# Performance work log

Measured on AMD Instinct MI355X. Metric: run time of the kernel, lower is better.

Reference implementation:

```python
import jax, jax.numpy as jnp
import numpy as np
from jax import lax

# Static configuration (matches init_kwargs / input_specs)
B, DIM, H, W = 4, 192, 64, 64
HEADS, SR, WS = 8, 4, 3
HD = DIM // HEADS            # 24
LL = WS * WS                 # 9  (local window length)
N = H * W                    # 4096 tokens
PH, PW = H // SR, W // SR    # 16, 16 pooled grid
PLEN = PH * PW               # 256
PRETRAIN = 512 // 8          # img_size // 2**(i+2) with i=1 -> 64


def _ln(x, g, b, eps=1e-5):
    m = x.mean(-1, keepdims=True)
    v = ((x - m) ** 2).mean(-1, keepdims=True)
    return (x - m) / jnp.sqrt(v + eps) * g + b


def _l2norm(x):
    n = jnp.sqrt(jnp.sum(x * x, -1, keepdims=True))
    return x / jnp.maximum(n, 1e-12)


def _build_static():
    # get_relative_position_cpb: adaptive 1d pool of arange gives key coords
    qh = np.arange(H, dtype=np.float64)
    qw = np.arange(W, dtype=np.float64)
    kh = qh.reshape(PH, SR).mean(-1)  # H divisible by SR -> uniform bins
    kw = qw.reshape(PW, SR).mean(-1)
    KH, KW = np.meshgrid(kh, kw, indexing='ij')
    QH, QW = np.meshgrid(qh, qw, indexing='ij')
    rel_h = (QH.reshape(-1)[:, None] - KH.reshape(-1)[None, :]) / (PRETRAIN - 1) * 8
    rel_w = (QW.reshape(-1)[:, None] - KW.reshape(-1)[None, :]) / (PRETRAIN - 1) * 8
    rel_hw = np.stack([rel_h, rel_w], -1).reshape(-1, 2)
    table, idx = np.unique(rel_hw, axis=0, return_inverse=True)
    table = np.sign(table) * np.log2(np.abs(table) + 1.0) / np.log2(8.0)
    # get_seqlen_and_mask: validity of each of the 9 neighbors per position
    hh, ww = np.meshgrid(np.arange(H), np.arange(W), indexing='ij')
    hh, ww = hh.reshape(-1), ww.reshape(-1)
    valid = np.stack([(hh + dh >= 0) & (hh + dh < H) & (ww + dw >= 0) & (ww + dw < W)
                      for dh in (-1, 0, 1) for dw in (-1, 0, 1)], -1)  # [N, 9]
    pad_mask = ~valid
    seq_scale = np.log(valid.sum(-1, keepdims=True).astype(np.float64) + PLEN).astype(np.float32)  # [N,1]
    return idx.reshape(-1).astype(np.int32), table.astype(np.float32), seq_scale, pad_mask


def setup_inputs() -> dict:
    key = jax.random.key(0)
    ks = jax.random.split(key, 12)
    f32 = jnp.float32

    def tn(k, shape, std=0.02):
        return jax.random.truncated_normal(k, -2.0, 2.0, shape, f32) * std

    rel_idx, table, seq_scale, pad_mask = _build_static()
    return dict(
        x=jax.random.normal(ks[0], (B, DIM, H, W), f32),
        pe_w=tn(ks[1], (DIM, DIM, 3, 3)),
        pe_b=jnp.zeros((DIM,), f32),
        pe_ln_g=jnp.ones((DIM,), f32), pe_ln_b=jnp.zeros((DIM,), f32),
        q_w=tn(ks[2], (DIM, DIM)), q_b=jnp.zeros((DIM,), f32),
        kv_w=tn(ks[3], (2 * DIM, DIM)), kv_b=jnp.zeros((2 * DIM,), f32),
        sr_w=tn(ks[4], (DIM, DIM)), sr_b=jnp.zeros((DIM,), f32),
        norm_g=jnp.ones((DIM,), f32), norm_b=jnp.zeros((DIM,), f32),
        cpb1_w=tn(ks[5], (512, 2), 0.1), cpb1_b=jnp.zeros((512,), f32),
        cpb2_w=tn(ks[6], (HEADS, 512), 0.05), cpb2_b=jnp.zeros((HEADS,), f32),
        rpb_local=tn(ks[7], (HEADS, LL), 0.0004),
        learnable_tokens=tn(ks[8], (HEADS, HD, LL)),
        learnable_bias=jnp.zeros((HEADS, 1, LL), f32),
        query_embedding=tn(ks[9], (HEADS, 1, HD)),
        temperature=jnp.full((HEADS, 1, 1), float(np.log(np.exp(1.0 / 0.24) - 1.0)), f32),
        proj_w=tn(ks[10], (DIM, DIM)), proj_b=jnp.zeros((DIM,), f32),
        out_ln_g=jnp.ones((DIM,), f32), out_ln_b=jnp.zeros((DIM,), f32),
        rel_idx=jnp.asarray(rel_idx),
        coords_table=jnp.asarray(table),
        seq_scale=jnp.asarray(seq_scale),
        pad_mask=jnp.asarray(pad_mask),
    )


def _forward(x, pe_w, pe_b, pe_ln_g, pe_ln_b, q_w, q_b, kv_w, kv_b, sr_w, sr_b,
             norm_g, norm_b, cpb1_w, cpb1_b, cpb2_w, cpb2_b, rpb_local,
             learnable_tokens, learnable_bias, query_embedding, temperature,
             proj_w, proj_b, out_ln_g, out_ln_b,
             rel_idx, coords_table, seq_scale, pad_mask):
    # OverlapPatchEmbed: 3x3 conv s1 p1 -> tokens -> LN
    xc = lax.conv_general_dilated(x, pe_w, (1, 1), ((1, 1), (1, 1)),
                                  dimension_numbers=('NCHW', 'OIHW', 'NCHW')) + pe_b[None, :, None, None]
    t = _ln(xc.reshape(B, DIM, N).transpose(0, 2, 1), pe_ln_g, pe_ln_b)  # [B,N,C]

    # queries
    q = t @ q_w.T + q_b
    q_norm = _l2norm(q.reshape(B, N, HEADS, HD).transpose(0, 2, 1, 3))   # [B,h,N,d]
    q_scaled = (q_norm + query_embedding[None]) * jax.nn.softplus(temperature)[None] * seq_scale

    # local KV via 3x3 neighborhood gather (torch nn.Unfold)
    kv = t @ kv_w.T + kv_b                                               # [B,N,2C]
    k_loc = _l2norm(kv[..., :DIM].reshape(B, N, HEADS, HD)).reshape(B, N, DIM)
    kv_map = jnp.concatenate([k_loc, kv[..., DIM:]], -1).transpose(0, 2, 1).reshape(B, 2 * DIM, H, W)
    p = jnp.pad(kv_map, ((0, 0), (0, 0), (1, 1), (1, 1)))
    neigh = jnp.stack([p[:, :, kh:kh + H, kw:kw + W] for kh in range(WS) for kw in range(WS)], 2)
    neigh = neigh.reshape(B, 2 * HEADS, HD, LL, N).transpose(0, 1, 4, 2, 3)  # [B,2h,N,d,9]
    k_local, v_local = neigh[:, :HEADS], neigh[:, HEADS:]
    attn_local = jnp.einsum('bhnd,bhndl->bhnl', q_scaled, k_local) + rpb_local[None, :, None, :]
    attn_local = jnp.where(pad_mask[None, None], -jnp.inf, attn_local)   # [B,h,N,9]

    # pooled global KV: 1x1 conv -> GELU -> adaptive avg pool -> LN -> kv
    x_map = t.transpose(0, 2, 1).reshape(B, DIM, H, W)
    sr_out = jax.nn.gelu(jnp.einsum('oc,bchw->bohw', sr_w, x_map) + sr_b[None, :, None, None],
                         approximate=False)
    pooled = sr_out.reshape(B, DIM, PH, SR, PW, SR).mean((3, 5)).reshape(B, DIM, PLEN).transpose(0, 2, 1)
    pooled = _ln(pooled, norm_g, norm_b)
    kv_p = (pooled @ kv_w.T + kv_b).reshape(B, PLEN, 2 * HEADS, HD).transpose(0, 2, 1, 3)
    k_pool, v_pool = kv_p[:, :HEADS], kv_p[:, HEADS:]

    # CPB relative position bias for the pooled branch
    cpb = jax.nn.relu(coords_table @ cpb1_w.T + cpb1_b) @ cpb2_w.T + cpb2_b  # [T,h]
    pool_bias = cpb.T[:, rel_idx].reshape(HEADS, N, PLEN)
    attn_pool = jnp.einsum('bhnd,bhmd->bhnm', q_scaled, _l2norm(k_pool)) + pool_bias[None]

    # joint softmax over local + pooled keys
    attn = jax.nn.softmax(jnp.concatenate([attn_local, attn_pool], -1), -1)
    a_loc, a_pool = attn[..., :LL], attn[..., LL:]

    w_loc = jnp.einsum('bhnd,hdl->bhnl', q_norm, learnable_tokens) + learnable_bias[None] + a_loc
    x_local = jnp.einsum('bhnl,bhndl->bhnd', w_loc, v_local)
    x_pool = jnp.einsum('bhnm,bhmd->bhnd', a_pool, v_pool)

    out = (x_local + x_pool).transpose(0, 2, 1, 3).reshape(B, N, DIM) @ proj_w.T + proj_b
    out = _ln(out, out_ln_g, out_ln_b)
    return out.transpose(0, 2, 1).reshape(B, DIM, H, W)


def reference(x, pe_w, pe_b, pe_ln_g, pe_ln_b, q_w, q_b, kv_w, kv_b, sr_w, sr_b,
              norm_g, norm_b, cpb1_w, cpb1_b, cpb2_w, cpb2_b, rpb_local,
              learnable_tokens, learnable_bias, query_embedding, temperature,
              proj_w, proj_b, out_ln_g, out_ln_b,
              rel_idx, coords_table, seq_scale, pad_mask):
    return _forward(x, pe_w, pe_b, pe_ln_g, pe_ln_b, q_w, q_b, kv_w, kv_b, sr_w, sr_b,
                    norm_g, norm_b, cpb1_w, cpb1_b, cpb2_w, cpb2_b, rpb_local,
                    learnable_tokens, learnable_bias, query_embedding, temperature,
                    proj_w, proj_b, out_ln_g, out_ln_b,
                    rel_idx, coords_table, seq_scale, pad_mask)
```

## Files before the change

### kernel.cpp

```cpp
#include <hip/hip_runtime.h>
#include <stdint.h>


__device__ __forceinline__ float b2f(unsigned short u) {
  return __uint_as_float(((unsigned)u) << 16);
}
__device__ __forceinline__ unsigned short f2b(float f) {
  unsigned x = __float_as_uint(f);
  return (unsigned short)((x + 0x7fffu + ((x >> 16) & 1u)) >> 16);
}

constexpr size_t OFF_T    = 0;
constexpr size_t OFF_KMAP = 3145728;
constexpr size_t OFF_QN   = 9437184;
constexpr size_t OFF_QS   = 12582912;
constexpr size_t OFF_CTX  = 15728640;
constexpr size_t OFF_POOL = 18874368;
constexpr size_t OFF_KP   = 19070976;
constexpr size_t OFF_VP   = 19267584;
constexpr size_t OFF_CPB  = 19464192;
constexpr size_t OFF_BIAS = 19595264;
constexpr size_t OFF_WTC  = OFF_CTX;
constexpr size_t OFF_QT   = OFF_CTX + 331776;
constexpr size_t OFF_KVT  = OFF_CTX + 368640;
constexpr size_t OFF_SRT  = OFF_CTX + 442368;
constexpr size_t OFF_PJT  = OFF_KMAP;

__global__ __launch_bounds__(256) void k_wt_all(
    const float* __restrict__ pw, const float* __restrict__ qw,
    const float* __restrict__ kvw, const float* __restrict__ srw,
    float* __restrict__ w) {
  int gb = blockIdx.x;
  int tid = threadIdx.x;
  if (gb < 1296) {
    int i = gb * 256 + tid;
    int j = i % 12;
    int t1 = i / 12;
    int p = t1 % 9;
    int t2 = t1 / 9;
    int ocb = t2 % 16;
    int ic = t2 / 16;
    int oc = ocb * 12 + j;
    w[OFF_WTC + i] = pw[(size_t)oc * 1728 + ic * 9 + p];
  } else if (gb < 1440) {
    int i = (gb - 1296) * 256 + tid;
    int o = i % 192, k = i / 192;
    w[OFF_QT + i] = qw[(size_t)o * 192 + k];
  } else if (gb < 1728) {
    int i = (gb - 1440) * 256 + tid;
    int o = i % 384, k = i / 384;
    w[OFF_KVT + i] = kvw[(size_t)o * 192 + k];
  } else {
    int i = (gb - 1728) * 256 + tid;
    int o = i % 192, k = i / 192;
    w[OFF_SRT + i] = srw[(size_t)o * 192 + k];
  }
}
__global__ __launch_bounds__(256) void k_wt_gen(const float* __restrict__ src,
                                                float* __restrict__ dst, int O, int K) {
  int i = blockIdx.x * 256 + threadIdx.x;
  if (i >= O * K) return;
  int o = i % O, k = i / O;
  dst[i] = src[(size_t)o * K + k];
}

__global__ __launch_bounds__(256) void k_conv(
    const float* __restrict__ x, const float* __restrict__ wtc,
    float* __restrict__ p0, float* __restrict__ p1, float* __restrict__ p2) {
  __shared__ float xl[8 * 6 * 66];
  const int tid = threadIdx.x;
  const int lane = tid & 63;
  const int wv = __builtin_amdgcn_readfirstlane(tid >> 6);
  const int h0 = blockIdx.x * 4;
  const int b = blockIdx.y;
  const int zz = blockIdx.z;
  const int obase = (zz & 3) * 48;
  const int ith = zz >> 2;
  const int icb = ith * 8;
  const int ocb = (zz & 3) * 4 + wv;
  const int ow = obase + wv * 12;

  float acc[4][12];
#pragma unroll
  for (int ro = 0; ro < 4; ++ro)
#pragma unroll
    for (int j = 0; j < 12; ++j) acc[ro][j] = 0.f;

  float xr[13];
  auto loadx = [&](int ic0) {
#pragma unroll
    for (int s = 0; s < 13; ++s) {
      int f = tid + s * 256;
      float v = 0.f;
      if (f < 3168) {
        int ii = f / 396;
        int rem = f - ii * 396;
        int r = rem / 66;
        int wp = rem - r * 66;
        int hh = h0 + r - 1, ww = wp - 1;
        if (hh >= 0 && hh < 64 && ww >= 0 && ww < 64)
          v = x[((size_t)(b * 192 + ic0 * 8 + ii) << 12) + (hh << 6) + ww];
      }
      xr[s] = v;
    }
  };
  loadx(icb);

  for (int i2 = 0; i2 < 8; ++i2) {
    const int ic0 = icb + i2;
    __syncthreads();
#pragma unroll
    for (int s = 0; s < 13; ++s) {
      int f = tid + s * 256;
      if (f < 3168) {
        int ii = f / 396;
        int rem = f - ii * 396;
        int r = rem / 66;
        int wp = rem - r * 66;
        xl[(ii * 6 + r) * 66 + wp] = xr[s];
      }
    }
    __syncthreads();
    if (i2 < 7) loadx(ic0 + 1);
#pragma unroll 1
    for (int ii = 0; ii < 8; ++ii) {
      const float* wb = wtc + ((size_t)((ic0 * 8 + ii) * 16 + ocb) * 9) * 12;
      float xv[6][3];
#pragma unroll
      for (int r6 = 0; r6 < 6; ++r6) {
        const float* xp = &xl[(ii * 6 + r6) * 66 + lane];
        xv[r6][0] = xp[0]; xv[r6][1] = xp[1]; xv[r6][2] = xp[2];
      }
#pragma unroll
      for (int kh = 0; kh < 3; ++kh) {
#pragma unroll
        for (int kw = 0; kw < 3; ++kw) {
          const float4* wp = (const float4*)(wb + (size_t)(kh * 3 + kw) * 12);
          float4 wA = wp[0], wB = wp[1], wC = wp[2];
#pragma unroll
          for (int ro = 0; ro < 4; ++ro) {
            float xvv = xv[ro + kh][kw];
            acc[ro][0]  += xvv * wA.x;
            acc[ro][1]  += xvv * wA.y;
            acc[ro][2]  += xvv * wA.z;
            acc[ro][3]  += xvv * wA.w;
            acc[ro][4]  += xvv * wB.x;
            acc[ro][5]  += xvv * wB.y;
            acc[ro][6]  += xvv * wB.z;
            acc[ro][7]  += xvv * wB.w;
            acc[ro][8]  += xvv * wC.x;
            acc[ro][9]  += xvv * wC.y;
            acc[ro][10] += xvv * wC.z;
            acc[ro][11] += xvv * wC.w;
          }
        }
      }
    }
  }
  float* tdst = (ith == 0) ? p0 : ((ith == 1) ? p1 : p2);
#pragma unroll
  for (int ro = 0; ro < 4; ++ro) {
    float* op = tdst + ((size_t)b * 4096 + (h0 + ro) * 64 + lane) * 192 + ow;
#pragma unroll
    for (int j4 = 0; j4 < 3; ++j4) {
      float4 v;
      v.x = acc[ro][j4 * 4 + 0];
      v.y = acc[ro][j4 * 4 + 1];
      v.z = acc[ro][j4 * 4 + 2];
      v.w = acc[ro][j4 * 4 + 3];
      ((float4*)op)[j4] = v;
    }
  }
}

__global__ __launch_bounds__(256) void k_ln_rows(float* __restrict__ data,
    const float* __restrict__ data2, const float* __restrict__ data3,
    const float* __restrict__ cbias,
    const float* __restrict__ g, const float* __restrict__ be, int rows) {
  int lane = threadIdx.x & 63;
  int wv = threadIdx.x >> 6;
  int row = blockIdx.x * 4 + wv;
  if (row >= rows) return;
  float* p = data + (size_t)row * 192;
  float v0 = p[lane], v1 = p[lane + 64], v2 = p[lane + 128];
  if (data2) {
    const float* q = data2 + (size_t)row * 192;
    v0 += q[lane]; v1 += q[lane + 64]; v2 += q[lane + 128];
  }
  if (data3) {
    const float* q = data3 + (size_t)row * 192;
    v0 += q[lane]; v1 += q[lane + 64]; v2 += q[lane + 128];
  }
  if (cbias) {
    v0 += cbias[lane]; v1 += cbias[lane + 64]; v2 += cbias[lane + 128];
  }
  float s = v0 + v1 + v2;
  float sq = v0 * v0 + v1 * v1 + v2 * v2;
#pragma unroll
  for (int m = 32; m >= 1; m >>= 1) {
    s += __shfl_xor(s, m, 64);
    sq += __shfl_xor(sq, m, 64);
  }
  float mean = s * (1.f / 192.f);
  float var = sq * (1.f / 192.f) - mean * mean;
  float rstd = rsqrtf(var + 1e-5f);
  p[lane]       = (v0 - mean) * rstd * g[lane]       + be[lane];
  p[lane + 64]  = (v1 - mean) * rstd * g[lane + 64]  + be[lane + 64];
  p[lane + 128] = (v2 - mean) * rstd * g[lane + 128] + be[lane + 128];
}

template <int OCB, typename GXV, typename GXD>
__device__ __forceinline__ void gemm_tiles(
    float* __restrict__ xs, int tid, int lane, int wv,
    const float* __restrict__ wt, int ostr, int obase,
    float (&acc)[OCB / 4], GXV gxv, GXD gxd) {
  constexpr int NW4 = OCB / 16;
  float xr[8];
  auto loadx = [&](int k0) {
#pragma unroll
    for (int s = 0; s < 8; ++s) xr[s] = gxv(k0, tid + s * 256);
  };
  loadx(0);
  for (int kt = 0; kt < 6; ++kt) {
    __syncthreads();
#pragma unroll
    for (int s = 0; s < 8; ++s) xs[gxd(tid + s * 256)] = xr[s];
    __syncthreads();
    if (kt < 5) loadx((kt + 1) * 32);
    const float* wbase = wt + (size_t)kt * 32 * ostr + obase + wv * (NW4 * 4);
#pragma unroll 4
    for (int kk = 0; kk < 32; ++kk) {
      float xv = xs[kk * 66 + lane];
      const float4* wrow = (const float4*)(wbase + (size_t)kk * ostr);
#pragma unroll
      for (int j4 = 0; j4 < NW4; ++j4) {
        float4 w4 = wrow[j4];
        acc[j4 * 4 + 0] += xv * w4.x;
        acc[j4 * 4 + 1] += xv * w4.y;
        acc[j4 * 4 + 2] += xv * w4.z;
        acc[j4 * 4 + 3] += xv * w4.w;
      }
    }
  }
}

__global__ __launch_bounds__(256) void k_q(
    const float* __restrict__ t, const float* __restrict__ qt, const float* __restrict__ qb,
    const float* __restrict__ qe, const float* __restrict__ tmp, const float* __restrict__ ss,
    float* __restrict__ qno, float* __restrict__ qso) {
  __shared__ float xs[32 * 66];
  const int tid = threadIdx.x;
  const int lane = tid & 63;
  const int wv = __builtin_amdgcn_readfirstlane(tid >> 6);
  const int n0 = blockIdx.x * 64;
  const int b = blockIdx.y;
  const int obase = blockIdx.z * 96;
  const int hh = blockIdx.z * 4 + wv;
  const int oc0 = obase + wv * 24;
  float acc[24];
#pragma unroll
  for (int j = 0; j < 24; ++j) acc[j] = 0.f;

  gemm_tiles<96>(xs, tid, lane, wv, qt, 192, obase, acc,
    [&](int k0, int f) {
      int nl = f >> 5, kk = f & 31;
      return t[((size_t)b * 4096 + n0 + nl) * 192 + k0 + kk];
    },
    [&](int f) { return (f & 31) * 66 + (f >> 5); });

  const int n = n0 + lane;
  float ssv = ss[n];
  float sumsq = 0.f;
#pragma unroll
  for (int d = 0; d < 24; ++d) {
    float v = acc[d] + qb[oc0 + d];
    sumsq += v * v;
  }
  float rn = 1.f / fmaxf(sqrtf(sumsq), 1e-12f);
  float sp = log1pf(__expf(tmp[hh]));
#pragma unroll
  for (int d = 0; d < 24; ++d) {
    float qv = (acc[d] + qb[oc0 + d]) * rn;
    size_t o = ((size_t)(b * 8 + hh) * 24 + d) * 4096 + n;
    qno[o] = qv;
    qso[o] = (qv + qe[hh * 24 + d]) * sp * ssv;
  }
}

__global__ __launch_bounds__(256) void k_kv(
    const float* __restrict__ t, const float* __restrict__ kvt, const float* __restrict__ kb_,
    float* __restrict__ kmap) {
  __shared__ float xs[32 * 66];
  const int tid = threadIdx.x;
  const int lane = tid & 63;
  const int wv = __builtin_amdgcn_readfirstlane(tid >> 6);
  const int n0 = blockIdx.x * 64;
  const int b = blockIdx.y;
  const int obase = blockIdx.z * 96;
  const int oc0 = obase + wv * 24;
  const int n = n0 + lane;
  float acc[24];
#pragma unroll
  for (int j = 0; j < 24; ++j) acc[j] = 0.f;

  gemm_tiles<96>(xs, tid, lane, wv, kvt, 384, obase, acc,
    [&](int k0, int f) {
      int nl = f >> 5, kk = f & 31;
      return t[((size_t)b * 4096 + n0 + nl) * 192 + k0 + kk];
    },
    [&](int f) { return (f & 31) * 66 + (f >> 5); });

  if (oc0 < 192) {
    float sumsq = 0.f;
#pragma unroll
    for (int d = 0; d < 24; ++d) {
      float v = acc[d] + kb_[oc0 + d];
      sumsq += v * v;
    }
    float rn = 1.f / fmaxf(sqrtf(sumsq), 1e-12f);
#pragma unroll
    for (int d = 0; d < 24; ++d)
      kmap[((size_t)b * 384 + oc0 + d) * 4096 + n] = (acc[d] + kb_[oc0 + d]) * rn;
  } else {
#pragma unroll
    for (int d = 0; d < 24; ++d)
      kmap[((size_t)b * 384 + oc0 + d) * 4096 + n] = acc[d] + kb_[oc0 + d];
  }
}

__device__ __forceinline__ float gelu_exact(float v) {
  float u = v * 0.70710678118654752f;
  float a = fabsf(u);
  float tt = 1.f / (1.f + 0.3275911f * a);
  float poly = ((((1.061405429f * tt - 1.453152027f) * tt + 1.421413741f) * tt
                 - 0.284496736f) * tt + 0.254829592f) * tt;
  float erfa = 1.f - poly * __expf(-a * a);
  float erfv = (u < 0.f) ? -erfa : erfa;
  return 0.5f * v * (1.f + erfv);
}

__global__ __launch_bounds__(256) void k_srpool(
    const float* __restrict__ t, const float* __restrict__ srt, const float* __restrict__ sb,
    float* __restrict__ pooled) {
  __shared__ float xs[32 * 66];
  const int tid = threadIdx.x;
  const int lane = tid & 63;
  const int wv = __builtin_amdgcn_readfirstlane(tid >> 6);
  const int wx = blockIdx.x & 3;
  const int obase = (blockIdx.x >> 2) * 48;
  const int ph = blockIdx.y;
  const int b = blockIdx.z;
  const int oc0 = obase + wv * 12;
  float acc[12];
#pragma unroll
  for (int j = 0; j < 12; ++j) acc[j] = 0.f;

  gemm_tiles<48>(xs, tid, lane, wv, srt, 192, obase, acc,
    [&](int k0, int f) {
      int pl = f >> 5, kk = f & 31;
      int row = (ph * 4 + (pl >> 4)) * 64 + wx * 16 + (pl & 15);
      return t[((size_t)b * 4096 + row) * 192 + k0 + kk];
    },
    [&](int f) { return (f & 31) * 66 + (f >> 5); });

#pragma unroll
  for (int j = 0; j < 12; ++j) {
    float gv = gelu_exact(acc[j] + sb[oc0 + j]);
    gv += __shfl_xor(gv, 1, 64);
    gv += __shfl_xor(gv, 2, 64);
    gv += __shfl_xor(gv, 16, 64);
    gv += __shfl_xor(gv, 32, 64);
    if ((lane & 51) == 0) {
      int cell = (lane >> 2) & 3;
      int p = ph * 16 + wx * 4 + cell;
      pooled[((size_t)b * 256 + p) * 192 + oc0 + j] = gv * (1.f / 16.f);
    }
  }
}

__global__ __launch_bounds__(256) void k_kvp(
    const float* __restrict__ pooled, const float* __restrict__ kvt, const float* __restrict__ kb_,
    float* __restrict__ kp, float* __restrict__ vp) {
  __shared__ float xs[32 * 66];
  const int tid = threadIdx.x;
  const int lane = tid & 63;
  const int wv = __builtin_amdgcn_readfirstlane(tid >> 6);
  const int r0 = blockIdx.x * 64;
  const int obase = blockIdx.y * 96;
  const int oc0 = obase + wv * 24;
  const int row = r0 + lane;
  const int b = row >> 8;
  const int m = row & 255;
  float acc[24];
#pragma unroll
  for (int j = 0; j < 24; ++j) acc[j] = 0.f;

  gemm_tiles<96>(xs, tid, lane, wv, kvt, 384, obase, acc,
    [&](int k0, int f) {
      int nl = f >> 5, kk = f & 31;
      return pooled[(size_t)(r0 + nl) * 192 + k0 + kk];
    },
    [&](int f) { return (f & 31) * 66 + (f >> 5); });

  if (oc0 < 192) {
    int hh = oc0 / 24;
    float sumsq = 0.f;
#pragma unroll
    for (int d = 0; d < 24; ++d) {
      float v = acc[d] + kb_[oc0 + d];
      sumsq += v * v;
    }
    float rn = 1.f / fmaxf(sqrtf(sumsq), 1e-12f);
#pragma unroll
    for (int d = 0; d < 24; ++d)
      kp[(((size_t)(b * 8 + hh)) * 256 + m) * 24 + d] = (acc[d] + kb_[oc0 + d]) * rn;
  } else {
    int hh = (oc0 - 192) / 24;
#pragma unroll
    for (int d = 0; d < 24; ++d)
      vp[(((size_t)(b * 8 + hh)) * 256 + m) * 24 + d] = acc[d] + kb_[oc0 + d];
  }
}

__global__ __launch_bounds__(256) void k_cpb(
    const float* __restrict__ coords, const float* __restrict__ c1w,
    const float* __restrict__ c1b, const float* __restrict__ c2w,
    const float* __restrict__ c2b, float* __restrict__ cpb, int T) {
  __shared__ float s1w[1024];
  __shared__ float s1b[512];
  __shared__ __align__(16) float s2w[512 * 8];
  const int tid = threadIdx.x;
  for (int f = tid; f < 1024; f += 256) s1w[f] = c1w[f];
  for (int f = tid; f < 512; f += 256) s1b[f] = c1b[f];
  for (int f = tid; f < 4096; f += 256) {
    int h = f >> 9, j = f & 511;
    s2w[j * 8 + h] = c2w[f];
  }
  __syncthreads();
  int i = blockIdx.x * 256 + tid;
  int ic = (i < T) ? i : (T - 1);
  float x0 = coords[2 * ic], y0 = coords[2 * ic + 1];
  float a[8];
#pragma unroll
  for (int h = 0; h < 8; ++h) a[h] = c2b[h];
#pragma unroll 4
  for (int j = 0; j < 512; ++j) {
    float hv = fmaxf(s1w[2 * j] * x0 + s1w[2 * j + 1] * y0 + s1b[j], 0.f);
    const float4* w2 = (const float4*)&s2w[j * 8];
    float4 wA = w2[0], wB = w2[1];
    a[0] += hv * wA.x; a[1] += hv * wA.y; a[2] += hv * wA.z; a[3] += hv * wA.w;
    a[4] += hv * wB.x; a[5] += hv * wB.y; a[6] += hv * wB.z; a[7] += hv * wB.w;
  }
  if (i < T) {
#pragma unroll
    for (int h = 0; h < 8; ++h) cpb[(size_t)i * 8 + h] = a[h];
  }
}

__global__ __launch_bounds__(256) void k_bias(
    const int* __restrict__ rel, const float* __restrict__ cpb,
    unsigned short* __restrict__ bt) {
  int g = blockIdx.x * 256 + threadIdx.x;
  int n = g >> 5;
  int m0 = (g & 31) * 8;
  const int4* r4 = (const int4*)(rel + (size_t)n * 256 + m0);
  int4 ra = r4[0], rb = r4[1];
  int idxs[8] = {ra.x, ra.y, ra.z, ra.w, rb.x, rb.y, rb.z, rb.w};
  unsigned acc[8][4];
#pragma unroll
  for (int j = 0; j < 8; ++j) {
    const float4* c4 = (const float4*)(cpb + (size_t)idxs[j] * 8);
    float4 A = c4[0], Bv = c4[1];
    float vals[8] = {A.x, A.y, A.z, A.w, Bv.x, Bv.y, Bv.z, Bv.w};
#pragma unroll
    for (int hh = 0; hh < 8; ++hh) {
      unsigned u = f2b(vals[hh]);
      if (j & 1) acc[hh][j >> 1] |= u << 16;
      else       acc[hh][j >> 1]  = u;
    }
  }
#pragma unroll
  for (int hh = 0; hh < 8; ++hh) {
    uint4 o;
    o.x = acc[hh][0]; o.y = acc[hh][1]; o.z = acc[hh][2]; o.w = acc[hh][3];
    *(uint4*)(bt + ((size_t)hh * 4096 + n) * 256 + m0) = o;
  }
}

__global__ __launch_bounds__(512, 4) void k_attn(
    const float* __restrict__ qs_g, const float* __restrict__ qn_g,
    const float* __restrict__ kmap, const float* __restrict__ kp, const float* __restrict__ vp,
    const unsigned short* __restrict__ bt, const float* __restrict__ rpb,
    const float* __restrict__ lt, const float* __restrict__ lb,
    float* __restrict__ ctx) {
  __shared__ __align__(16) float smem[12288];
  float* kl = smem;
  float* vl = smem + 6144;
  const int tid = threadIdx.x;
  const int lane = tid & 63;
  const int w = __builtin_amdgcn_readfirstlane(tid >> 6);
  const int qm = w & 3;
  const int rr = w >> 2;
  const int row = blockIdx.x * 2 + rr;
  const int h = blockIdx.y;
  const int b = blockIdx.z;
  const int n = (row << 6) + lane;
  const float SHIFT = 15.f;

  {
    const float4* kps = (const float4*)(kp + (size_t)(b * 8 + h) * 6144);
    const float4* vps = (const float4*)(vp + (size_t)(b * 8 + h) * 6144);
    float4* kld = (float4*)kl;
    float4* vld = (float4*)vl;
#pragma unroll
    for (int c = 0; c < 3; ++c) {
      int f = tid + c * 512;
      kld[f] = kps[f];
      vld[f] = vps[f];
    }
  }

  float qsv[24];
  {
    const float* qsb = qs_g + ((size_t)(b * 8 + h) * 24) * 4096 + n;
#pragma unroll
    for (int d = 0; d < 24; ++d) qsv[d] = qsb[(size_t)d * 4096];
  }

  const int l0 = (qm == 1) ? 0 : ((qm == 0) ? 3 : (qm * 2 + 1));
  const int lcnt = (qm == 1) ? 3 : 2;

  float wlv[3];
  {
    float qnv[24];
    const float* qnb = qn_g + ((size_t)(b * 8 + h) * 24) * 4096 + n;
#pragma unroll
    for (int d = 0; d < 24; ++d) qnv[d] = qnb[(size_t)d * 4096];
    const float* ltp = lt + h * 216;
    const float* lbp = lb + h * 9;
#pragma unroll
    for (int j = 0; j < 3; ++j) {
      float a = 0.f;
      if (j < lcnt) {
        int l = l0 + j;
#pragma unroll
        for (int d = 0; d < 24; ++d) a += qnv[d] * ltp[d * 9 + l];
        a += lbp[l];
      }
      wlv[j] = a;
    }
  }

  float ctxA[24], ctxBP[24];
#pragma unroll
  for (int d = 0; d < 24; ++d) { ctxA[d] = 0.f; ctxBP[d] = 0.f; }
  float S = 0.f;

  {
    const float* kbase = kmap + ((size_t)b * 384 + h * 24) * 4096;
    const float* rpp = rpb + h * 9;
    for (int j = 0; j < lcnt; ++j) {
      const int l = l0 + j;
      const int dh = l / 3 - 1, dw = l % 3 - 1;
      const int hp = row + dh;
      if (hp < 0 || hp >= 64) continue;
      const int wp2 = lane + dw;
      const bool okw = (wp2 >= 0) && (wp2 < 64);
      const int nn = (hp << 6) + (okw ? wp2 : lane);
      const float* kb = kbase + nn;
      const float* vb = kb + (size_t)192 * 4096;
      float d0 = 0, d1 = 0, d2 = 0, d3 = 0;
#pragma unroll
      for (int d = 0; d < 24; d += 4) {
        d0 += qsv[d] * kb[(size_t)d * 4096];
        d1 += qsv[d + 1] * kb[(size_t)(d + 1) * 4096];
        d2 += qsv[d + 2] * kb[(size_t)(d + 2) * 4096];
        d3 += qsv[d + 3] * kb[(size_t)(d + 3) * 4096];
      }
      float p = okw ? __expf((d0 + d1) + (d2 + d3) + rpp[l] - SHIFT) : 0.f;
      S += p;
      float wll = okw ? wlv[j] : 0.f;
#pragma unroll
      for (int d = 0; d < 24; ++d) {
        float vv = vb[(size_t)d * 4096];
        ctxA[d] += wll * vv;
        ctxBP[d] += p * vv;
      }
    }
  }

  __syncthreads();

  {
    const unsigned short* bp = bt + ((size_t)h * 4096 + n) * 256 + qm * 64;
    const float* klq = kl + qm * (64 * 24);
    const float* vlq = vl + qm * (64 * 24);
    uint4 bcur = *(const uint4*)bp;
#pragma unroll 1
    for (int c = 0; c < 8; ++c) {
      uint4 bnx = bcur;
      if (c < 7) bnx = *(const uint4*)(bp + (c + 1) * 8);
#pragma unroll
      for (int j = 0; j < 8; ++j) {
        const float4* kr4 = (const float4*)&klq[(c * 8 + j) * 24];
        const float4* vr4 = (const float4*)&vlq[(c * 8 + j) * 24];
        float d0 = 0, d1 = 0, d2 = 0, d3 = 0;
#pragma unroll
        for (int q4 = 0; q4 < 6; ++q4) {
          float4 k4 = kr4[q4];
          d0 += qsv[q4 * 4 + 0] * k4.x;
          d1 += qsv[q4 * 4 + 1] * k4.y;
          d2 += qsv[q4 * 4 + 2] * k4.z;
          d3 += qsv[q4 * 4 + 3] * k4.w;
        }
        unsigned word = (j < 2) ? bcur.x : (j < 4) ? bcur.y : (j < 6) ? bcur.z : bcur.w;
        float bv = (j & 1) ? __uint_as_float(word & 0xffff0000u)
                           : __uint_as_float(word << 16);
        float p = __expf((d0 + d1) + (d2 + d3) + bv - SHIFT);
        S += p;
#pragma unroll
        for (int q4 = 0; q4 < 6; ++q4) {
          float4 v4 = vr4[q4];
          ctxBP[q4 * 4 + 0] += p * v4.x;
          ctxBP[q4 * 4 + 1] += p * v4.y;
          ctxBP[q4 * 4 + 2] += p * v4.z;
          ctxBP[q4 * 4 + 3] += p * v4.w;
        }
      }
      bcur = bnx;
    }
  }

  for (int src = 1; src < 4; ++src) {
    __syncthreads();
    if (qm == src) {
      float* p = smem + (size_t)(rr * 64 + lane) * 49;
      p[0] = S;
#pragma unroll
      for (int d = 0; d < 24; ++d) { p[1 + d] = ctxA[d]; p[25 + d] = ctxBP[d]; }
    }
    __syncthreads();
    if (qm == 0) {
      const float* p = smem + (size_t)(rr * 64 + lane) * 49;
      S += p[0];
#pragma unroll
      for (int d = 0; d < 24; ++d) { ctxA[d] += p[1 + d]; ctxBP[d] += p[25 + d]; }
    }
  }
  if (qm == 0) {
    const float inv = 1.f / S;
    float* cb = ctx + ((size_t)(b * 8 + h) * 24) * 4096 + n;
#pragma unroll
    for (int d = 0; d < 24; ++d)
      cb[(size_t)d * 4096] = ctxA[d] + ctxBP[d] * inv;
  }
}

__global__ __launch_bounds__(256) void k_projg(
    const float* __restrict__ ctx, const float* __restrict__ pjt, const float* __restrict__ pb,
    float* __restrict__ pout) {
  __shared__ float xs[32 * 66];
  const int tid = threadIdx.x;
  const int lane = tid & 63;
  const int wv = __builtin_amdgcn_readfirstlane(tid >> 6);
  const int n0 = blockIdx.x * 64;
  const int b = blockIdx.y;
  const int obase = blockIdx.z * 96;
  const int oc0 = obase + wv * 24;
  const int n = n0 + lane;
  float acc[24];
#pragma unroll
  for (int j = 0; j < 24; ++j) acc[j] = 0.f;

  gemm_tiles<96>(xs, tid, lane, wv, pjt, 192, obase, acc,
    [&](int k0, int f) {
      int kk = f >> 6, nl = f & 63;
      return ctx[((size_t)b * 192 + k0 + kk) * 4096 + n0 + nl];
    },
    [&](int f) { return (f >> 6) * 66 + (f & 63); });

#pragma unroll
  for (int d = 0; d < 24; ++d)
    pout[((size_t)b * 192 + oc0 + d) * 4096 + n] = acc[d] + pb[oc0 + d];
}

__global__ __launch_bounds__(256) void k_oln(
    const float* __restrict__ pout, const float* __restrict__ g,
    const float* __restrict__ be, float* __restrict__ out) {
  __shared__ float red[2][4][64];
  const int tid = threadIdx.x;
  const int lane = tid & 63;
  const int wv = __builtin_amdgcn_readfirstlane(tid >> 6);
  const int n0 = blockIdx.x * 64;
  const int b = blockIdx.y;
  const int o0 = wv * 48;
  float v[48];
  float s = 0.f, sq = 0.f;
#pragma unroll
  for (int j = 0; j < 48; ++j) {
    v[j] = pout[((size_t)b * 192 + o0 + j) * 4096 + n0 + lane];
    s += v[j];
    sq += v[j] * v[j];
  }
  red[0][wv][lane] = s;
  red[1][wv][lane] = sq;
  __syncthreads();
  float st = red[0][0][lane] + red[0][1][lane] + red[0][2][lane] + red[0][3][lane];
  float sqt = red[1][0][lane] + red[1][1][lane] + red[1][2][lane] + red[1][3][lane];
  float mean = st * (1.f / 192.f);
  float var = sqt * (1.f / 192.f) - mean * mean;
  float rstd = rsqrtf(var + 1e-5f);
#pragma unroll
  for (int j = 0; j < 48; ++j) {
    int o = o0 + j;
    out[((size_t)b * 192 + o) * 4096 + n0 + lane] = (v[j] - mean) * rstd * g[o] + be[o];
  }
}

extern "C" void kernel_launch(void* const* d_in, const int* in_sizes, int n_in,
                              void* d_out, int out_size, void* d_ws, size_t ws_size,
                              hipStream_t stream) {
  float* w = (float*)d_ws;

  const float* x      = (const float*)d_in[0];
  const float* pe_w   = (const float*)d_in[1];
  const float* pe_b   = (const float*)d_in[2];
  const float* peln_g = (const float*)d_in[3];
  const float* peln_b = (const float*)d_in[4];
  const float* q_w    = (const float*)d_in[5];
  const float* q_b    = (const float*)d_in[6];
  const float* kv_w   = (const float*)d_in[7];
  const float* kv_b   = (const float*)d_in[8];
  const float* sr_w   = (const float*)d_in[9];
  const float* sr_b   = (const float*)d_in[10];
  const float* norm_g = (const float*)d_in[11];
  const float* norm_b = (const float*)d_in[12];
  const float* cpb1w  = (const float*)d_in[13];
  const float* cpb1b  = (const float*)d_in[14];
  const float* cpb2w  = (const float*)d_in[15];
  const float* cpb2b  = (const float*)d_in[16];
  const float* rpb    = (const float*)d_in[17];
  const float* lt     = (const float*)d_in[18];
  const float* lb     = (const float*)d_in[19];
  const float* qe     = (const float*)d_in[20];
  const float* temp   = (const float*)d_in[21];
  const float* proj_w = (const float*)d_in[22];
  const float* proj_b = (const float*)d_in[23];
  const float* oln_g  = (const float*)d_in[24];
  const float* oln_b  = (const float*)d_in[25];
  const int*   rel    = (const int*)d_in[26];
  const float* coords = (const float*)d_in[27];
  const float* ss     = (const float*)d_in[28];

  dim3 blk(256);
  k_wt_all<<<dim3(1872), blk, 0, stream>>>(pe_w, q_w, kv_w, sr_w, w);

  k_conv<<<dim3(16, 4, 12), blk, 0, stream>>>(x, w + OFF_WTC, w + OFF_T,
      w + OFF_KMAP, w + OFF_KMAP + 3145728);
  k_ln_rows<<<dim3(4096), blk, 0, stream>>>(w + OFF_T, w + OFF_KMAP,
      w + OFF_KMAP + 3145728, pe_b, peln_g, peln_b, 16384);
  k_q<<<dim3(64, 4, 2), blk, 0, stream>>>(w + OFF_T, w + OFF_QT, q_b, qe, temp, ss,
      w + OFF_QN, w + OFF_QS);
  k_kv<<<dim3(64, 4, 4), blk, 0, stream>>>(w + OFF_T, w + OFF_KVT, kv_b, w + OFF_KMAP);
  k_srpool<<<dim3(16, 16, 4), blk, 0, stream>>>(w + OFF_T, w + OFF_SRT, sr_b, w + OFF_POOL);
  k_ln_rows<<<dim3(256), blk, 0, stream>>>(w + OFF_POOL, nullptr, nullptr, nullptr,
      norm_g, norm_b, 1024);
  k_kvp<<<dim3(16, 4), blk, 0, stream>>>(w + OFF_POOL, w + OFF_KVT, kv_b,
      w + OFF_KP, w + OFF_VP);
  int T = in_sizes[27] / 2;
  k_cpb<<<dim3((T + 255) / 256), blk, 0, stream>>>(coords, cpb1w, cpb1b, cpb2w, cpb2b,
      w + OFF_CPB, T);
  k_bias<<<dim3(512), blk, 0, stream>>>(rel, w + OFF_CPB,
      (unsigned short*)(w + OFF_BIAS));
  k_attn<<<dim3(32, 8, 4), dim3(512), 0, stream>>>(w + OFF_QS, w + OFF_QN, w + OFF_KMAP,
      w + OFF_KP, w + OFF_VP, (const unsigned short*)(w + OFF_BIAS), rpb, lt, lb,
      w + OFF_CTX);
  k_wt_gen<<<dim3(144), blk, 0, stream>>>(proj_w, w + OFF_PJT, 192, 192);
  k_projg<<<dim3(64, 4, 2), blk, 0, stream>>>(w + OFF_CTX, w + OFF_PJT, proj_b,
      w + OFF_QN);
  k_oln<<<dim3(64, 4), blk, 0, stream>>>(w + OFF_QN, oln_g, oln_b, (float*)d_out);
}
```

Measured before the change: 546.9 us.

## Fuse output projection with LayerNorm and relayout conv weights to oc-contiguous

Merges the output projection GEMM and the final LayerNorm into one 512-thread kernel, so each block computes all 192 output channels for 64 tokens and normalises them in registers. This removes the intermediate projection write and read-back and one launch. Separately, the patch-embed conv weight transpose now stores weights as [ic*9+p][oc], and the conv kernel indexes with a 192 stride. The fused kernel runs half as many blocks, each twice as large, which may lower occupancy.

```diff
diff --git a/kernel.cpp b/kernel.cpp
--- a/kernel.cpp
+++ b/kernel.cpp
@@ -34,14 +34,8 @@
   int tid = threadIdx.x;
   if (gb < 1296) {
     int i = gb * 256 + tid;
-    int j = i % 12;
-    int t1 = i / 12;
-    int p = t1 % 9;
-    int t2 = t1 / 9;
-    int ocb = t2 % 16;
-    int ic = t2 / 16;
-    int oc = ocb * 12 + j;
-    w[OFF_WTC + i] = pw[(size_t)oc * 1728 + ic * 9 + p];
+    int oc = i % 192, k = i / 192;
+    w[OFF_WTC + i] = pw[(size_t)oc * 1728 + k];
   } else if (gb < 1440) {
     int i = (gb - 1296) * 256 + tid;
     int o = i % 192, k = i / 192;
@@ -77,7 +71,6 @@
   const int obase = (zz & 3) * 48;
   const int ith = zz >> 2;
   const int icb = ith * 8;
-  const int ocb = (zz & 3) * 4 + wv;
   const int ow = obase + wv * 12;
 
   float acc[4][12];
@@ -122,9 +115,9 @@
     }
     __syncthreads();
     if (i2 < 7) loadx(ic0 + 1);
+    const float* wb = wtc + (size_t)ic0 * 72 * 192 + ow;
 #pragma unroll 1
     for (int ii = 0; ii < 8; ++ii) {
-      const float* wb = wtc + ((size_t)((ic0 * 8 + ii) * 16 + ocb) * 9) * 12;
       float xv[6][3];
 #pragma unroll
       for (int r6 = 0; r6 < 6; ++r6) {
@@ -135,7 +128,7 @@
       for (int kh = 0; kh < 3; ++kh) {
 #pragma unroll
         for (int kw = 0; kw < 3; ++kw) {
-          const float4* wp = (const float4*)(wb + (size_t)(kh * 3 + kw) * 12);
+          const float4* wp = (const float4*)(wb + (size_t)(ii * 9 + kh * 3 + kw) * 192);
           float4 wA = wp[0], wB = wp[1], wC = wp[2];
 #pragma unroll
           for (int ro = 0; ro < 4; ++ro) {
@@ -656,64 +649,80 @@
   }
 }
 
-__global__ __launch_bounds__(256) void k_projg(
+__global__ __launch_bounds__(512) void k_projoln(
     const float* __restrict__ ctx, const float* __restrict__ pjt, const float* __restrict__ pb,
-    float* __restrict__ pout) {
+    const float* __restrict__ g, const float* __restrict__ be, float* __restrict__ out) {
   __shared__ float xs[32 * 66];
+  __shared__ float red[2][8][64];
   const int tid = threadIdx.x;
   const int lane = tid & 63;
   const int wv = __builtin_amdgcn_readfirstlane(tid >> 6);
   const int n0 = blockIdx.x * 64;
   const int b = blockIdx.y;
-  const int obase = blockIdx.z * 96;
-  const int oc0 = obase + wv * 24;
-  const int n = n0 + lane;
+  const int oc0 = wv * 24;
   float acc[24];
 #pragma unroll
   for (int j = 0; j < 24; ++j) acc[j] = 0.f;
 
-  gemm_tiles<96>(xs, tid, lane, wv, pjt, 192, obase, acc,
-    [&](int k0, int f) {
+  float xr[4];
+  auto loadx = [&](int k0) {
+#pragma unroll
+    for (int s = 0; s < 4; ++s) {
+      int f = tid + s * 512;
       int kk = f >> 6, nl = f & 63;
-      return ctx[((size_t)b * 192 + k0 + kk) * 4096 + n0 + nl];
-    },
-    [&](int f) { return (f >> 6) * 66 + (f & 63); });
-
-#pragma unroll
-  for (int d = 0; d < 24; ++d)
-    pout[((size_t)b * 192 + oc0 + d) * 4096 + n] = acc[d] + pb[oc0 + d];
-}
-
-__global__ __launch_bounds__(256) void k_oln(
-    const float* __restrict__ pout, const float* __restrict__ g,
-    const float* __restrict__ be, float* __restrict__ out) {
-  __shared__ float red[2][4][64];
-  const int tid = threadIdx.x;
-  const int lane = tid & 63;
-  const int wv = __builtin_amdgcn_readfirstlane(tid >> 6);
-  const int n0 = blockIdx.x * 64;
-  const int b = blockIdx.y;
-  const int o0 = wv * 48;
-  float v[48];
+      xr[s] = ctx[((size_t)b * 192 + k0 + kk) * 4096 + n0 + nl];
+    }
+  };
+  loadx(0);
+  for (int kt = 0; kt < 6; ++kt) {
+    __syncthreads();
+#pragma unroll
+    for (int s = 0; s < 4; ++s) {
+      int f = tid + s * 512;
+      xs[(f >> 6) * 66 + (f & 63)] = xr[s];
+    }
+    __syncthreads();
+    if (kt < 5) loadx((kt + 1) * 32);
+    const float* wbase = pjt + (size_t)kt * 32 * 192 + oc0;
+#pragma unroll 4
+    for (int kk = 0; kk < 32; ++kk) {
+      float xv = xs[kk * 66 + lane];
+      const float4* wrow = (const float4*)(wbase + (size_t)kk * 192);
+#pragma unroll
+      for (int j4 = 0; j4 < 6; ++j4) {
+        float4 w4 = wrow[j4];
+        acc[j4 * 4 + 0] += xv * w4.x;
+        acc[j4 * 4 + 1] += xv * w4.y;
+        acc[j4 * 4 + 2] += xv * w4.z;
+        acc[j4 * 4 + 3] += xv * w4.w;
+      }
+    }
+  }
+
+  float v[24];
   float s = 0.f, sq = 0.f;
 #pragma unroll
-  for (int j = 0; j < 48; ++j) {
-    v[j] = pout[((size_t)b * 192 + o0 + j) * 4096 + n0 + lane];
-    s += v[j];
-    sq += v[j] * v[j];
+  for (int d = 0; d < 24; ++d) {
+    v[d] = acc[d] + pb[oc0 + d];
+    s += v[d];
+    sq += v[d] * v[d];
   }
   red[0][wv][lane] = s;
   red[1][wv][lane] = sq;
   __syncthreads();
-  float st = red[0][0][lane] + red[0][1][lane] + red[0][2][lane] + red[0][3][lane];
-  float sqt = red[1][0][lane] + red[1][1][lane] + red[1][2][lane] + red[1][3][lane];
+  float st = 0.f, sqt = 0.f;
+#pragma unroll
+  for (int k = 0; k < 8; ++k) {
+    st += red[0][k][lane];
+    sqt += red[1][k][lane];
+  }
   float mean = st * (1.f / 192.f);
   float var = sqt * (1.f / 192.f) - mean * mean;
   float rstd = rsqrtf(var + 1e-5f);
 #pragma unroll
-  for (int j = 0; j < 48; ++j) {
-    int o = o0 + j;
-    out[((size_t)b * 192 + o) * 4096 + n0 + lane] = (v[j] - mean) * rstd * g[o] + be[o];
+  for (int d = 0; d < 24; ++d) {
+    int o = oc0 + d;
+    out[((size_t)b * 192 + o) * 4096 + n0 + lane] = (v[d] - mean) * rstd * g[o] + be[o];
   }
 }
 
@@ -776,7 +785,6 @@
       w + OFF_KP, w + OFF_VP, (const unsigned short*)(w + OFF_BIAS), rpb, lt, lb,
       w + OFF_CTX);
   k_wt_gen<<<dim3(144), blk, 0, stream>>>(proj_w, w + OFF_PJT, 192, 192);
-  k_projg<<<dim3(64, 4, 2), blk, 0, stream>>>(w + OFF_CTX, w + OFF_PJT, proj_b,
-      w + OFF_QN);
-  k_oln<<<dim3(64, 4), blk, 0, stream>>>(w + OFF_QN, oln_g, oln_b, (float*)d_out);
-}
+  k_projoln<<<dim3(64, 4), dim3(512), 0, stream>>>(w + OFF_CTX, w + OFF_PJT, proj_b,
+      oln_g, oln_b, (float*)d_out);
+}
```

New measurement: 520.0 us. -4.9%, faster.
